# Optimization experiments

Measured on AMD Instinct MI355X. Metric: run time of the kernel, lower is better.

The kernel has to match this reference:

```python
import jax, jax.numpy as jnp
import numpy as np

HIDDEN = 128
N_RBF = 32
LMAX = 2
N_NODES = 10000
DEG = 8  # each node has DEG outgoing (and DEG incoming) edges on a ring


def _build_graph():
    src = np.repeat(np.arange(N_NODES, dtype=np.int64), DEG)
    offs = np.tile(np.arange(1, DEG + 1, dtype=np.int64), N_NODES)
    dst = (src + offs) % N_NODES
    keys = src * N_NODES + dst
    order = np.argsort(keys)
    src2, dst2 = src[order], dst[order]  # e2 sorted by key (searchsorted invariant)
    e1_to_e2 = np.empty_like(order)
    e1_to_e2[order] = np.arange(order.size)
    return src, dst, src2, dst2, e1_to_e2


def setup_inputs() -> dict:
    key = jax.random.key(0)
    ks = jax.random.split(key, 12)
    src1, dst1, src2, dst2, e1_to_e2 = _build_graph()
    E1, E2 = src1.size, src2.size
    in_dim = 6 * HIDDEN + 3 * N_RBF + 1  # 865

    def lin(k, fi, fo):
        kw, kb = jax.random.split(k)
        s = 1.0 / np.sqrt(fi)
        return (jax.random.uniform(kw, (fi, fo), minval=-s, maxval=s),
                jax.random.uniform(kb, (fo,), minval=-s, maxval=s))

    w1, b1 = lin(ks[0], in_dim, HIDDEN)
    w2, b2 = lin(ks[1], HIDDEN, HIDDEN)
    wgw, bgw = lin(ks[2], HIDDEN, HIDDEN)
    wgt, bgt = lin(ks[3], HIDDEN, HIDDEN)
    return {
        "t_e2": jax.random.normal(ks[4], (E2, HIDDEN), dtype=jnp.float32),
        "h": jax.random.normal(ks[5], (N_NODES, HIDDEN), dtype=jnp.float32),
        "edge_index1": jnp.asarray(np.stack([src1, dst1])),
        "edge_index2": jnp.asarray(np.stack([src2, dst2])),
        "e1_to_e2": jnp.asarray(e1_to_e2),
        "dist_e1": jax.random.uniform(ks[6], (E1,), dtype=jnp.float32),
        "dist_e2": jax.random.uniform(ks[7], (E2,), dtype=jnp.float32),
        "rbf_e1": jax.random.normal(ks[8], (E1, N_RBF), dtype=jnp.float32),
        "rbf_e2": jax.random.normal(ks[9], (E2, N_RBF), dtype=jnp.float32),
        "sph_e1": jax.random.normal(ks[10], (E1, LMAX + 1), dtype=jnp.float32),
        "num_nodes": N_NODES,
        "w1": w1, "b1": b1, "w2": w2, "b2": b2,
        "wgw": wgw, "bgw": bgw, "wgt": wgt, "bgt": bgt,
    }


def _wedge_indices(edge_index1, edge_index2, num_nodes):
    """Host-side (numpy, vectorized) wedge construction: for every center node k,
    all (incoming edge i->k, outgoing edge k->j) pairs with i != j, kept only when
    (i, j) itself is an edge in e2 (looked up by sorted key search)."""
    src1 = np.asarray(edge_index1[0]); dst1 = np.asarray(edge_index1[1])
    src2 = np.asarray(edge_index2[0]); dst2 = np.asarray(edge_index2[1])
    nz = src1 != dst1  # drop self-loops
    s, d = src1[nz], dst1[nz]
    eid = np.nonzero(nz)[0]
    out_deg = np.bincount(s, minlength=num_nodes)
    out_order = np.argsort(s, kind="stable")  # filtered-edge positions grouped by src
    out_ptr = np.concatenate([np.zeros(1, np.int64), np.cumsum(out_deg)])
    reps = out_deg[d]  # each incoming edge pairs with out_deg[center] outgoing edges
    total = int(reps.sum())
    if total == 0:
        z = np.zeros(0, np.int64)
        return z, z, z, z, z, z
    starts = np.cumsum(reps) - reps
    local = np.arange(total) - np.repeat(starts, reps)
    kj_f = out_order[np.repeat(out_ptr[d], reps) + local]
    i = np.repeat(s, reps)
    k = np.repeat(d, reps)
    eik = np.repeat(eid, reps)
    j = d[kj_f]
    ekj = eid[kj_f]
    m = i != j
    i, k, j, eik, ekj = i[m], k[m], j[m], eik[m], ekj[m]
    e2_keys = src2.astype(np.int64) * num_nodes + dst2
    pk = i.astype(np.int64) * num_nodes + j
    pos = np.searchsorted(e2_keys, pk)
    posc = np.minimum(pos, e2_keys.size - 1)
    valid = (pos < e2_keys.size) & (e2_keys[posc] == pk)
    return i[valid], k[valid], j[valid], eik[valid], ekj[valid], posc[valid]


def reference(t_e2, h, edge_index1, edge_index2, e1_to_e2, dist_e1, dist_e2,
              rbf_e1, rbf_e2, sph_e1, num_nodes,
              w1, b1, w2, b2, wgw, bgw, wgt, bgt):
    i, k, j, eik, ekj, eij = _wedge_indices(edge_index1, edge_index2, int(num_nodes))
    if i.size == 0:
        return t_e2
    i, k, j = jnp.asarray(i), jnp.asarray(k), jnp.asarray(j)
    eik, ekj, eij = jnp.asarray(eik), jnp.asarray(ekj), jnp.asarray(eij)
    e1e2 = jnp.asarray(e1_to_e2)
    # wedge geometric features (wedge_use_high_degree=False -> l=1 contraction only)
    c_feat = (sph_e1[eik, 1] * sph_e1[ekj, 1])[:, None]           # [W, 1]
    g = jnp.concatenate([rbf_e1[eik], rbf_e1[ekj], rbf_e2[eij], c_feat], axis=-1)
    rho_in = jnp.concatenate([t_e2[e1e2[eik]], t_e2[e1e2[ekj]], t_e2[eij],
                              h[i], h[k], h[j], g], axis=-1)       # [W, 865]
    msg = jax.nn.silu(rho_in @ w1 + b1) @ w2 + b2                  # [W, H]
    m = jax.ops.segment_sum(msg, eij, num_segments=t_e2.shape[0])  # [E2, H]
    return t_e2 + jax.nn.sigmoid(m @ wgw + bgw) * jnp.tanh(t_e2 @ wgt + bgt)
```

## Files before the change

kernel.cpp:

```cpp
#include <hip/hip_runtime.h>
#include <math.h>

typedef unsigned short u16;
typedef unsigned int u32;
typedef __bf16 bf16x8 __attribute__((ext_vector_type(8)));
typedef float f32x4 __attribute__((ext_vector_type(4)));

__device__ __forceinline__ float bf2f(u16 v){ union{u32 u;float f;}c; c.u=((u32)v)<<16; return c.f; }
__device__ __forceinline__ u16 f2bf(float f){ union{float f;u32 u;}c; c.f=f; u32 l=(c.u>>16)&1u; c.u+=0x7fffu+l; return (u16)(c.u>>16); }
__device__ __forceinline__ u32 pk2(float a, float b){ return (u32)f2bf(a) | ((u32)f2bf(b)<<16); }
__device__ __forceinline__ uint4 ld8f(const float* p){
  float4 x = ((const float4*)p)[0];
  float4 y = ((const float4*)p)[1];
  uint4 r; r.x=pk2(x.x,x.y); r.y=pk2(x.z,x.w); r.z=pk2(y.x,y.y); r.w=pk2(y.z,y.w);
  return r;
}
__device__ __forceinline__ float fsilu(float x){ return x/(1.f+__expf(-x)); }

__device__ __forceinline__ void async16(const u16* g, u16* l) {
  __builtin_amdgcn_global_load_lds(
      (const __attribute__((address_space(1))) u32*)(g),
      (__attribute__((address_space(3))) u32*)(l), 16, 0, 0);
}

struct SArgs {
  const float *t, *h, *r2, *rbf_e1, *sph_e1, *w1, *w2, *wgw, *wgt, *b2;
  const int *e1_to_e2, *src2;
  u16 *T16, *h16, *rbf2b, *rbf1p, *WbigT, *WcT, *WgtT;
  float *sph_c, *bc2;
  int *out_ptr, *cnt;
  long n_t, n_h, n_r;
  int E1, E2, Nn;
  int B0, B1, B2, B3, B4, B5;
};

__global__ __launch_bounds__(256)
void k_setup(SArgs s) {
  int b = blockIdx.x, tid = threadIdx.x;
  if (b < s.B0) {
    long base = ((long)b*256 + tid)*8;
    if (base < s.n_t) {
      *(uint4*)(s.T16+base) = ld8f(s.t+base);
    } else if (base < s.n_t+s.n_h) {
      long o = base-s.n_t;  *(uint4*)(s.h16+o) = ld8f(s.h+o);
    } else if (base < s.n_t+s.n_h+s.n_r) {
      long o = base-s.n_t-s.n_h; *(uint4*)(s.rbf2b+o) = ld8f(s.r2+o);
    }
  } else if (b < s.B1) {
    int e = (b-s.B0)*256 + tid;
    if (e < s.E1) {
      int f = s.e1_to_e2[e];
      s.sph_c[f] = s.sph_e1[e*3+1];
      const float* src = s.rbf_e1 + (size_t)e*32;
      uint4* d = (uint4*)(s.rbf1p + (size_t)f*32);
      d[0]=ld8f(src); d[1]=ld8f(src+8); d[2]=ld8f(src+16); d[3]=ld8f(src+24);
    }
  } else if (b < s.B2) {
    int n = (b-s.B1)*256 + tid;
    if (n <= s.Nn) {
      int lo=0, hi=s.E2;
      while (lo<hi){ int m=(lo+hi)>>1; if (s.src2[m]<n) lo=m+1; else hi=m; }
      s.out_ptr[n]=lo;
    }
  } else if (b < s.B3) {
    int id = (b-s.B2)*256 + tid;
    if (id < 384*448) {
      int n = id/448, k = id%448;
      int q = n>>7, nn = n&127;
      int row = -1;
      if (k<128) row = q*128+k;
      else if (k<256) { if (q==0) row = 384+(k-128); }
      else if (k<384) { if (q==0) row = 512+(k-256); else if (q==1) row = 640+(k-256); }
      else if (k<416) { if (q==0) row = 768+(k-384); else if (q==1) row = 800+(k-384); }
      else { if (q==2) row = 832+(k-416); }
      s.WbigT[id] = (row>=0) ? f2bf(s.w1[row*128+nn]) : (u16)0;
    }
  } else if (b < s.B4) {
    int id = (b-s.B3)*256 + tid;
    if (id < 16384) {
      int n = id&127, k = id>>7;
      float acc = 0.f;
      for (int r=0;r<128;r++) acc += s.w2[k*128+r]*s.wgw[r*128+n];
      s.WcT[n*128+k] = f2bf(acc);
      s.WgtT[n*128+k] = f2bf(s.wgt[k*128+n]);
    } else if (id < 16384+128) {
      int n = id-16384;
      float acc = 0.f;
      for (int r=0;r<128;r++) acc += s.b2[r]*s.wgw[r*128+n];
      s.bc2[n] = acc;
    }
  } else if (b < s.B5) {
    int e = (b-s.B4)*256 + tid;
    if (e < s.E2) s.cnt[e] = 0;
  }
}

__global__ __launch_bounds__(256, 8)
void k_enum(const int* __restrict__ src2, const int* __restrict__ dst2,
            const int* __restrict__ out_ptr, const float* __restrict__ sph_c,
            int4* __restrict__ wrec, int* __restrict__ cnt, int E2) {
  int id = blockIdx.x*256 + threadIdx.x;
  if (id >= E2*8) return;
  int gw = id >> 3, d = id & 7;
  int i = src2[gw], j = dst2[gw];
  int f = out_ptr[i] + d;
  if (f >= out_ptr[i+1]) return;
  int k = dst2[f];
  int lo = out_ptr[k], hi = out_ptr[k+1], hi0 = hi;
  while (lo<hi) { int m=(lo+hi)>>1; if (dst2[m]<j) lo=m+1; else hi=m; }
  if (lo < hi0 && dst2[lo]==j) {
    float cf = sph_c[f]*sph_c[lo];
    int slot = atomicAdd(&cnt[gw], 1);
    int4 r; r.x=f; r.y=lo; r.z=__float_as_int(cf); r.w=0;
    wrec[(size_t)gw*8 + slot] = r;
  }
}

__global__ __launch_bounds__(256, 8)
void k_wedge2(const u16* __restrict__ Q1, const u16* __restrict__ Q2,
              const u16* __restrict__ P3, const int4* __restrict__ wrec,
              const int* __restrict__ cnt, const float* __restrict__ w1,
              u16* __restrict__ S, int E2) {
  int gw = (int)((blockIdx.x*256 + threadIdx.x) >> 6);
  int lane = threadIdx.x & 63;
  if (gw >= E2) return;
  u32 p3u = ((const u32*)(P3 + (size_t)gw*128))[lane];
  float p30 = bf2f((u16)(p3u&0xffff)), p31 = bf2f((u16)(p3u>>16));
  float2 wv = ((const float2*)(w1 + 864*128))[lane];
  const u32* q1b = (const u32*)Q1;
  const u32* q2b = (const u32*)Q2;
  const int4* wr = wrec + (size_t)gw*8;
  int c = cnt[gw];
  float a0=0.f, a1=0.f;
  int w = 0;
  for (; w+2<=c; w+=2) {
    int4 rA = wr[w], rB = wr[w+1];
    u32 xA = q1b[(size_t)rA.x*64 + lane];
    u32 yA = q2b[(size_t)rA.y*64 + lane];
    u32 xB = q1b[(size_t)rB.x*64 + lane];
    u32 yB = q2b[(size_t)rB.y*64 + lane];
    float cfA = __int_as_float(rA.z), cfB = __int_as_float(rB.z);
    float x0 = p30 + bf2f((u16)(xA&0xffff)) + bf2f((u16)(yA&0xffff)) + cfA*wv.x;
    float x1 = p31 + bf2f((u16)(xA>>16))    + bf2f((u16)(yA>>16))    + cfA*wv.y;
    float z0 = p30 + bf2f((u16)(xB&0xffff)) + bf2f((u16)(yB&0xffff)) + cfB*wv.x;
    float z1 = p31 + bf2f((u16)(xB>>16))    + bf2f((u16)(yB>>16))    + cfB*wv.y;
    a0 += fsilu(x0) + fsilu(z0);
    a1 += fsilu(x1) + fsilu(z1);
  }
  if (w < c) {
    int4 rA = wr[w];
    u32 xA = q1b[(size_t)rA.x*64 + lane];
    u32 yA = q2b[(size_t)rA.y*64 + lane];
    float cfA = __int_as_float(rA.z);
    float x0 = p30 + bf2f((u16)(xA&0xffff)) + bf2f((u16)(yA&0xffff)) + cfA*wv.x;
    float x1 = p31 + bf2f((u16)(xA>>16))    + bf2f((u16)(yA>>16))    + cfA*wv.y;
    a0 += fsilu(x0);
    a1 += fsilu(x1);
  }
  ((u32*)(S + (size_t)gw*128))[lane] = pk2(a0, a1);
}

struct GArgs {
  const u16 *T16, *h16, *rbf1p, *rbf2b, *Asrc;
  const int *src2, *dst2, *cnt;
  const u16 *Bmat, *Bmat2;
  const float *b1, *bgw, *bgt, *bc2;
  u16 *out0, *out1, *out2;
  float* outf;
  int M;
};

template<int MODE>
__global__ __launch_bounds__(256, 2)
void k_gemm(GArgs a) {
  constexpr int NK = (MODE==0)?14:8;
  constexpr int NA = (MODE==0)?1:2;
  __shared__ u16 As[2][4096];
  __shared__ u16 Bs[2][4096];
  const int tid = threadIdx.x;
  const int bm = blockIdx.x, bn = (MODE==0)? blockIdx.y : 0;
  const int lane = tid & 63, wave = tid >> 6;
  const int wm = wave >> 1, wn = wave & 1;
  const int quad = lane >> 4, l16 = lane & 15;

  const int ar = (wave & 1)*64 + lane;
  const int qh = wave >> 1;
  long fa = (long)bm*128 + ar;
  if (fa >= a.M) fa = a.M-1;

  const u16 *tb, *hs, *hd, *r1, *r2;
  if constexpr (MODE==0) {
    int sa = a.src2[fa], da = a.dst2[fa];
    tb = a.T16 + fa*128; hs = a.h16 + (long)sa*128; hd = a.h16 + (long)da*128;
    r1 = a.rbf1p + fa*32; r2 = a.rbf2b + fa*32;
  } else {
    tb = a.Asrc + fa*128;
    hs = a.T16 + fa*128;
  }
  auto agp = [&](int ks, int q) -> const u16* {
    if constexpr (MODE==0) {
      if (ks<4)   return tb + ks*32 + q*8;
      if (ks<8)   return hs + (ks-4)*32 + q*8;
      if (ks<12)  return hd + (ks-8)*32 + q*8;
      if (ks==12) return r1 + q*8;
      return r2 + q*8;
    } else {
      if (ks<4) return tb + ks*32 + q*8;
      return hs + (ks-4)*32 + q*8;
    }
  };
  const u16* Bb0; const u16* Bb1 = nullptr;
  if constexpr (MODE==0) { Bb0 = a.Bmat + (long)(bn*128 + ar)*448; }
  else { Bb0 = a.Bmat + (long)ar*128; Bb1 = a.Bmat2 + (long)ar*128; }
  auto bgp = [&](int ks, int q) -> const u16* {
    if constexpr (MODE==0) return Bb0 + ks*32 + q*8;
    else return (ks<4) ? (Bb0 + ks*32 + q*8) : (Bb1 + (ks-4)*32 + q*8);
  };
  auto issue = [&](int ks, int buf) {
    async16(agp(ks, qh),   As[buf] + wave*512);
    async16(agp(ks, qh+2), As[buf] + (4+wave)*512);
    async16(bgp(ks, qh),   Bs[buf] + wave*512);
    async16(bgp(ks, qh+2), Bs[buf] + (4+wave)*512);
  };

  issue(0, 0);
  __syncthreads();

  f32x4 acc[NA][4][4] = {};
  for (int ks=0; ks<NK; ks++) {
    const int buf = ks & 1;
    if (ks+1 < NK) issue(ks+1, buf^1);
    const int sel = (NA==2) ? (ks>>2) : 0;
    bf16x8 af[4], bfr[4];
    #pragma unroll
    for (int t=0;t<4;t++) {
      af[t]  = *(const bf16x8*)(As[buf] + quad*1024 + (wm*64 + t*16 + l16)*8);
      bfr[t] = *(const bf16x8*)(Bs[buf] + quad*1024 + (wn*64 + t*16 + l16)*8);
    }
    #pragma unroll
    for (int tm=0;tm<4;tm++)
      #pragma unroll
      for (int tn=0;tn<4;tn++)
        acc[sel][tm][tn] = __builtin_amdgcn_mfma_f32_16x16x32_bf16(af[tm], bfr[tn], acc[sel][tm][tn], 0,0,0);
    __syncthreads();
  }

  #pragma unroll
  for (int tm=0;tm<4;tm++) {
    const int rloc = wm*64 + tm*16 + quad*4;
    #pragma unroll
    for (int r=0;r<4;r++) {
      long row = (long)bm*128 + rloc + r;
      if (row >= a.M) continue;
      #pragma unroll
      for (int tn=0;tn<4;tn++) {
        const int col = wn*64 + tn*16 + l16;
        if constexpr (MODE==0) {
          float v = acc[0][tm][tn][r];
          u16* dst = (bn==0)? a.out0 : (bn==1)? a.out1 : a.out2;
          if (bn==2) v += a.b1[col];
          dst[row*128 + col] = f2bf(v);
        } else {
          float u = acc[0][tm][tn][r] + (float)a.cnt[row]*a.bc2[col] + a.bgw[col];
          float g = 1.f/(1.f+__expf(-u));
          float vv = acc[1][tm][tn][r] + a.bgt[col];
          float th = 1.f - 2.f/(__expf(2.f*vv)+1.f);
          float t  = bf2f(a.T16[row*128+col]);
          a.outf[row*128+col] = t + g*th;
        }
      }
    }
  }
}

extern "C" void kernel_launch(void* const* d_in, const int* in_sizes, int n_in,
                              void* d_out, int out_size, void* d_ws, size_t ws_size,
                              hipStream_t stream) {
  const float* t_e2  = (const float*)d_in[0];
  const float* h     = (const float*)d_in[1];
  const int* ei2     = (const int*)d_in[3];
  const int* e1_to_e2 = (const int*)d_in[4];
  const float* rbf_e1 = (const float*)d_in[7];
  const float* rbf_e2 = (const float*)d_in[8];
  const float* sph_e1 = (const float*)d_in[9];
  const float* w1  = (const float*)d_in[11];
  const float* b1  = (const float*)d_in[12];
  const float* w2  = (const float*)d_in[13];
  const float* b2  = (const float*)d_in[14];
  const float* wgw = (const float*)d_in[15];
  const float* bgw = (const float*)d_in[16];
  const float* wgt = (const float*)d_in[17];
  const float* bgt = (const float*)d_in[18];

  const int E2 = in_sizes[0]/128;
  const int Nn = in_sizes[1]/128;
  const int E1 = in_sizes[5];
  const int* src2 = ei2;
  const int* dst2 = ei2 + E2;

  char* p = (char*)d_ws;
  u16* Q1 = (u16*)p;       p += (size_t)E2*128*2;
  u16* Q2 = (u16*)p;       p += (size_t)E2*128*2;
  u16* P3 = (u16*)p;       p += (size_t)E2*128*2;
  u16* T16 = (u16*)p;      p += (size_t)E2*128*2;
  u16* h16 = (u16*)p;      p += (size_t)Nn*128*2;
  u16* rbf2b = (u16*)p;    p += (size_t)E2*32*2;
  u16* rbf1p = (u16*)p;    p += (size_t)E2*32*2;
  u16* WbigT = (u16*)p;    p += (size_t)384*448*2;
  u16* WcT   = (u16*)p;    p += (size_t)128*128*2;
  u16* WgtT  = (u16*)p;    p += (size_t)128*128*2;
  float* sph_c = (float*)p; p += (size_t)E2*4;
  float* bc2   = (float*)p; p += 512;
  int* out_ptr = (int*)p;   p += (((size_t)(Nn+1)*4 + 63)/64)*64;
  int* cnt     = (int*)p;   p += (size_t)E2*4;
  int4* wrec   = (int4*)p;  p += (size_t)E2*8*16;
  u16* S = P3;

  long n_t = (long)E2*128, n_h = (long)Nn*128, n_r = (long)E2*32;
  long tot8 = (n_t+n_h+n_r)/8;

  SArgs s;
  s.t=t_e2; s.h=h; s.r2=rbf_e2; s.rbf_e1=rbf_e1; s.sph_e1=sph_e1;
  s.w1=w1; s.w2=w2; s.wgw=wgw; s.wgt=wgt; s.b2=b2;
  s.e1_to_e2=e1_to_e2; s.src2=src2;
  s.T16=T16; s.h16=h16; s.rbf2b=rbf2b; s.rbf1p=rbf1p;
  s.WbigT=WbigT; s.WcT=WcT; s.WgtT=WgtT;
  s.sph_c=sph_c; s.bc2=bc2; s.out_ptr=out_ptr; s.cnt=cnt;
  s.n_t=n_t; s.n_h=n_h; s.n_r=n_r; s.E1=E1; s.E2=E2; s.Nn=Nn;
  int B0 = (int)((tot8+255)/256);
  int B1 = B0 + (E1+255)/256;
  int B2 = B1 + (Nn+1+255)/256;
  int B3 = B2 + (384*448+255)/256;
  int B4 = B3 + (16512+255)/256;
  int B5 = B4 + (E2+255)/256;
  s.B0=B0; s.B1=B1; s.B2=B2; s.B3=B3; s.B4=B4; s.B5=B5;
  k_setup<<<B5, 256, 0, stream>>>(s);

  k_enum<<<(E2*8+255)/256, 256, 0, stream>>>(src2, dst2, out_ptr, sph_c, wrec, cnt, E2);

  const int Mb = (E2+127)/128;
  {
    GArgs a = {};
    a.T16=T16; a.h16=h16; a.rbf1p=rbf1p; a.rbf2b=rbf2b;
    a.src2=src2; a.dst2=dst2; a.Bmat=WbigT; a.b1=b1;
    a.out0=Q1; a.out1=Q2; a.out2=P3; a.M=E2;
    k_gemm<0><<<dim3(Mb,3), 256, 0, stream>>>(a);
  }
  k_wedge2<<<(E2+3)/4, 256, 0, stream>>>(Q1, Q2, P3, wrec, cnt, w1, S, E2);
  {
    GArgs a = {};
    a.Asrc=S; a.T16=T16; a.cnt=cnt; a.Bmat=WcT; a.Bmat2=WgtT;
    a.bgw=bgw; a.bgt=bgt; a.bc2=bc2;
    a.outf=(float*)d_out; a.M=E2;
    k_gemm<1><<<dim3(Mb,1), 256, 0, stream>>>(a);
  }
}
```

Baseline: 340.1 us.

## Replace tail GEMM template with dedicated 64-row direct-load gate kernel

```diff
diff --git a/kernel.cpp b/kernel.cpp
--- a/kernel.cpp
+++ b/kernel.cpp
@@ -161,24 +161,21 @@
 }
 
 struct GArgs {
-  const u16 *T16, *h16, *rbf1p, *rbf2b, *Asrc;
-  const int *src2, *dst2, *cnt;
-  const u16 *Bmat, *Bmat2;
-  const float *b1, *bgw, *bgt, *bc2;
+  const u16 *T16, *h16, *rbf1p, *rbf2b;
+  const int *src2, *dst2;
+  const u16 *Bmat;
+  const float *b1;
   u16 *out0, *out1, *out2;
-  float* outf;
   int M;
 };
 
-template<int MODE>
 __global__ __launch_bounds__(256, 2)
-void k_gemm(GArgs a) {
-  constexpr int NK = (MODE==0)?14:8;
-  constexpr int NA = (MODE==0)?1:2;
+void k_gemm0(GArgs a) {
+  constexpr int NK = 14;
   __shared__ u16 As[2][4096];
   __shared__ u16 Bs[2][4096];
   const int tid = threadIdx.x;
-  const int bm = blockIdx.x, bn = (MODE==0)? blockIdx.y : 0;
+  const int bm = blockIdx.x, bn = blockIdx.y;
   const int lane = tid & 63, wave = tid >> 6;
   const int wm = wave >> 1, wn = wave & 1;
   const int quad = lane >> 4, l16 = lane & 15;
@@ -188,49 +185,34 @@
   long fa = (long)bm*128 + ar;
   if (fa >= a.M) fa = a.M-1;
 
-  const u16 *tb, *hs, *hd, *r1, *r2;
-  if constexpr (MODE==0) {
-    int sa = a.src2[fa], da = a.dst2[fa];
-    tb = a.T16 + fa*128; hs = a.h16 + (long)sa*128; hd = a.h16 + (long)da*128;
-    r1 = a.rbf1p + fa*32; r2 = a.rbf2b + fa*32;
-  } else {
-    tb = a.Asrc + fa*128;
-    hs = a.T16 + fa*128;
-  }
+  int sa = a.src2[fa], da = a.dst2[fa];
+  const u16* tb = a.T16 + fa*128;
+  const u16* hs = a.h16 + (long)sa*128;
+  const u16* hd = a.h16 + (long)da*128;
+  const u16* r1 = a.rbf1p + fa*32;
+  const u16* r2 = a.rbf2b + fa*32;
   auto agp = [&](int ks, int q) -> const u16* {
-    if constexpr (MODE==0) {
-      if (ks<4)   return tb + ks*32 + q*8;
-      if (ks<8)   return hs + (ks-4)*32 + q*8;
-      if (ks<12)  return hd + (ks-8)*32 + q*8;
-      if (ks==12) return r1 + q*8;
-      return r2 + q*8;
-    } else {
-      if (ks<4) return tb + ks*32 + q*8;
-      return hs + (ks-4)*32 + q*8;
-    }
+    if (ks<4)   return tb + ks*32 + q*8;
+    if (ks<8)   return hs + (ks-4)*32 + q*8;
+    if (ks<12)  return hd + (ks-8)*32 + q*8;
+    if (ks==12) return r1 + q*8;
+    return r2 + q*8;
   };
-  const u16* Bb0; const u16* Bb1 = nullptr;
-  if constexpr (MODE==0) { Bb0 = a.Bmat + (long)(bn*128 + ar)*448; }
-  else { Bb0 = a.Bmat + (long)ar*128; Bb1 = a.Bmat2 + (long)ar*128; }
-  auto bgp = [&](int ks, int q) -> const u16* {
-    if constexpr (MODE==0) return Bb0 + ks*32 + q*8;
-    else return (ks<4) ? (Bb0 + ks*32 + q*8) : (Bb1 + (ks-4)*32 + q*8);
-  };
+  const u16* Bb0 = a.Bmat + (long)(bn*128 + ar)*448;
   auto issue = [&](int ks, int buf) {
-    async16(agp(ks, qh),   As[buf] + wave*512);
-    async16(agp(ks, qh+2), As[buf] + (4+wave)*512);
-    async16(bgp(ks, qh),   Bs[buf] + wave*512);
-    async16(bgp(ks, qh+2), Bs[buf] + (4+wave)*512);
+    async16(agp(ks, qh),        As[buf] + wave*512);
+    async16(agp(ks, qh+2),      As[buf] + (4+wave)*512);
+    async16(Bb0 + ks*32 + qh*8,     Bs[buf] + wave*512);
+    async16(Bb0 + ks*32 + (qh+2)*8, Bs[buf] + (4+wave)*512);
   };
 
   issue(0, 0);
   __syncthreads();
 
-  f32x4 acc[NA][4][4] = {};
+  f32x4 acc[4][4] = {};
   for (int ks=0; ks<NK; ks++) {
     const int buf = ks & 1;
     if (ks+1 < NK) issue(ks+1, buf^1);
-    const int sel = (NA==2) ? (ks>>2) : 0;
     bf16x8 af[4], bfr[4];
     #pragma unroll
     for (int t=0;t<4;t++) {
@@ -241,7 +223,7 @@
     for (int tm=0;tm<4;tm++)
       #pragma unroll
       for (int tn=0;tn<4;tn++)
-        acc[sel][tm][tn] = __builtin_amdgcn_mfma_f32_16x16x32_bf16(af[tm], bfr[tn], acc[sel][tm][tn], 0,0,0);
+        acc[tm][tn] = __builtin_amdgcn_mfma_f32_16x16x32_bf16(af[tm], bfr[tn], acc[tm][tn], 0,0,0);
     __syncthreads();
   }
 
@@ -255,19 +237,66 @@
       #pragma unroll
       for (int tn=0;tn<4;tn++) {
         const int col = wn*64 + tn*16 + l16;
-        if constexpr (MODE==0) {
-          float v = acc[0][tm][tn][r];
-          u16* dst = (bn==0)? a.out0 : (bn==1)? a.out1 : a.out2;
-          if (bn==2) v += a.b1[col];
-          dst[row*128 + col] = f2bf(v);
-        } else {
-          float u = acc[0][tm][tn][r] + (float)a.cnt[row]*a.bc2[col] + a.bgw[col];
-          float g = 1.f/(1.f+__expf(-u));
-          float vv = acc[1][tm][tn][r] + a.bgt[col];
-          float th = 1.f - 2.f/(__expf(2.f*vv)+1.f);
-          float t  = bf2f(a.T16[row*128+col]);
-          a.outf[row*128+col] = t + g*th;
-        }
+        float v = acc[tm][tn][r];
+        u16* dst = (bn==0)? a.out0 : (bn==1)? a.out1 : a.out2;
+        if (bn==2) v += a.b1[col];
+        dst[row*128 + col] = f2bf(v);
+      }
+    }
+  }
+}
+
+__global__ __launch_bounds__(256, 4)
+void k_tail(const u16* __restrict__ S, const u16* __restrict__ T16,
+            const u16* __restrict__ WcT, const u16* __restrict__ WgtT,
+            const int* __restrict__ cnt, const float* __restrict__ bc2,
+            const float* __restrict__ bgw, const float* __restrict__ bgt,
+            float* __restrict__ outf, int M) {
+  const int tid = threadIdx.x;
+  const int lane = tid & 63, wave = tid >> 6;
+  const int quad = lane >> 4, l16 = lane & 15;
+  const long r0 = (long)blockIdx.x*64;
+
+  f32x4 acc[2][4][2] = {};
+  #pragma unroll
+  for (int ks=0; ks<8; ks++) {
+    const int sel = ks>>2, kb = (ks&3)*32;
+    const u16* Ab = sel ? T16 : S;
+    const u16* Bb = sel ? WgtT : WcT;
+    bf16x8 av[4], bv[2];
+    #pragma unroll
+    for (int tm=0;tm<4;tm++) {
+      long row = r0 + tm*16 + l16; if (row >= M) row = M-1;
+      av[tm] = *(const bf16x8*)(Ab + row*128 + kb + quad*8);
+    }
+    #pragma unroll
+    for (int tn=0;tn<2;tn++) {
+      int col = wave*32 + tn*16 + l16;
+      bv[tn] = *(const bf16x8*)(Bb + (long)col*128 + kb + quad*8);
+    }
+    #pragma unroll
+    for (int tm=0;tm<4;tm++)
+      #pragma unroll
+      for (int tn=0;tn<2;tn++)
+        acc[sel][tm][tn] = __builtin_amdgcn_mfma_f32_16x16x32_bf16(av[tm], bv[tn], acc[sel][tm][tn], 0,0,0);
+  }
+
+  #pragma unroll
+  for (int tm=0;tm<4;tm++) {
+    #pragma unroll
+    for (int r=0;r<4;r++) {
+      long row = r0 + tm*16 + quad*4 + r;
+      if (row >= M) continue;
+      float cn = (float)cnt[row];
+      #pragma unroll
+      for (int tn=0;tn<2;tn++) {
+        int col = wave*32 + tn*16 + l16;
+        float u = acc[0][tm][tn][r] + cn*bc2[col] + bgw[col];
+        float g = 1.f/(1.f+__expf(-u));
+        float vv = acc[1][tm][tn][r] + bgt[col];
+        float th = 1.f - 2.f/(__expf(2.f*vv)+1.f);
+        float t = bf2f(T16[row*128+col]);
+        outf[row*128+col] = t + g*th;
       }
     }
   }
@@ -344,14 +373,11 @@
     a.T16=T16; a.h16=h16; a.rbf1p=rbf1p; a.rbf2b=rbf2b;
     a.src2=src2; a.dst2=dst2; a.Bmat=WbigT; a.b1=b1;
     a.out0=Q1; a.out1=Q2; a.out2=P3; a.M=E2;
-    k_gemm<0><<<dim3(Mb,3), 256, 0, stream>>>(a);
+    k_gemm0<<<dim3(Mb,3), 256, 0, stream>>>(a);
   }
   k_wedge2<<<(E2+3)/4, 256, 0, stream>>>(Q1, Q2, P3, wrec, cnt, w1, S, E2);
-  {
-    GArgs a = {};
-    a.Asrc=S; a.T16=T16; a.cnt=cnt; a.Bmat=WcT; a.Bmat2=WgtT;
-    a.bgw=bgw; a.bgt=bgt; a.bc2=bc2;
-    a.outf=(float*)d_out; a.M=E2;
-    k_gemm<1><<<dim3(Mb,1), 256, 0, stream>>>(a);
-  }
-}
+
+  const int Mb64 = (E2+63)/64;
+  k_tail<<<Mb64, 256, 0, stream>>>(S, T16, WcT, WgtT, cnt, bc2, bgw, bgt,
+                                   (float*)d_out, E2);
+}
```

Result: no change. 336.9 us (-0.9%).
